# Optimization experiments

Measured on AMD Instinct MI355X. Metric: run time of the kernel, lower is better.

## Reference

```python
import jax, jax.numpy as jnp
import numpy as np

N_NODES = 100000
N_EDGES = 3200000
N_FEAT = 128
N_HID = 128
N_CLASS = 16
AVG_DEG = 32


def setup_inputs() -> dict:
    key = jax.random.key(0)
    ks = jax.random.split(key, 8)
    x = jax.random.normal(ks[0], (N_NODES, N_FEAT), dtype=jnp.float32)
    edge_row = jax.random.randint(ks[1], (N_EDGES,), 0, N_NODES, dtype=jnp.int32)
    edge_col = jax.random.randint(ks[2], (N_EDGES,), 0, N_NODES, dtype=jnp.int32)
    # normalized adjacency values ~ 1/degree
    edge_val = jax.random.uniform(ks[3], (N_EDGES,), dtype=jnp.float32) * (1.0 / AVG_DEG)
    W1 = jax.random.normal(ks[4], (N_FEAT, N_HID), dtype=jnp.float32) * (1.0 / np.sqrt(N_FEAT))
    b1 = jnp.zeros((N_HID,), dtype=jnp.float32)
    W4 = jax.random.normal(ks[5], (N_HID, N_CLASS), dtype=jnp.float32) * (1.0 / np.sqrt(N_HID))
    b4 = jnp.zeros((N_CLASS,), dtype=jnp.float32)
    return {"x": x, "edge_val": edge_val, "W1": W1, "b1": b1, "W4": W4, "b4": b4,
            "edge_row": edge_row, "edge_col": edge_col}


def _spmm(edge_val, edge_row, edge_col, feats, n_nodes):
    # sparse adj (COO) @ dense feats: gather source rows, scale, scatter-add to dest rows
    msgs = edge_val[:, None] * feats[edge_col]  # [E, D]
    return jax.ops.segment_sum(msgs, edge_row, num_segments=n_nodes)


def reference(x, edge_val, W1, b1, W4, b4, edge_row, edge_col):
    # gc1: adj @ (x @ W1) + b1, then ReLU (dropout is identity in eval mode)
    h = jax.nn.relu(_spmm(edge_val, edge_row, edge_col, x @ W1, N_NODES) + b1)
    # gc4: adj @ (h @ W4) + b4
    out = _spmm(edge_val, edge_row, edge_col, h @ W4, N_NODES) + b4
    return jax.nn.log_softmax(out, axis=1)
```

## Files before the change

### kernel.cpp

```cpp
#include <hip/hip_runtime.h>
#include <hip/hip_bf16.h>

constexpr int NN = 100000;
constexpr int NE = 3200000;
constexpr int NWG = 256;
constexpr int CHUNK = NE / NWG;
constexpr int CHUNK4 = CHUNK / 4;
constexpr int NBUK1 = (NN + 511) / 512;

__device__ __forceinline__ unsigned short f2bf(float f) {
    unsigned int u = __float_as_uint(f);
    unsigned int r = (u + 0x7fffu + ((u >> 16) & 1u)) >> 16;
    return (unsigned short)r;
}

__global__ __launch_bounds__(256) void k_gemm1(const float* __restrict__ x,
                                               const float* __restrict__ W,
                                               unsigned short* __restrict__ y) {
    __shared__ float ws_[128 * 128];
    __shared__ float xs[8][128];
    const int t = threadIdx.x;
    for (int i = t; i < 128 * 128; i += 256) ws_[i] = W[i];

    const int rowg = t >> 5;
    const int cq   = (t & 31) * 4;
    const int row0 = blockIdx.x * 32;

    for (int rs = 0; rs < 32; rs += 8) {
        __syncthreads();
        {
            const int r  = t >> 5;
            const int c4 = (t & 31) * 4;
            const int row = row0 + rs + r;
            float4 val = (row < NN) ? *(const float4*)(x + row * 128 + c4)
                                    : make_float4(0.f, 0.f, 0.f, 0.f);
            *(float4*)(&xs[r][c4]) = val;
        }
        __syncthreads();
        float4 acc = make_float4(0.f, 0.f, 0.f, 0.f);
#pragma unroll
        for (int k = 0; k < 128; ++k) {
            const float xv = xs[rowg][k];
            const float4 wv = *(const float4*)(&ws_[k * 128 + cq]);
            acc.x = fmaf(xv, wv.x, acc.x);
            acc.y = fmaf(xv, wv.y, acc.y);
            acc.z = fmaf(xv, wv.z, acc.z);
            acc.w = fmaf(xv, wv.w, acc.w);
        }
        const int row = row0 + rs + rowg;
        if (row < NN) {
            ushort4 o;
            o.x = f2bf(acc.x); o.y = f2bf(acc.y);
            o.z = f2bf(acc.z); o.w = f2bf(acc.w);
            *(ushort4*)(y + row * 128 + cq) = o;
        }
    }
}


__global__ __launch_bounds__(256) void k_count(const int4* __restrict__ erow4,
                                               int* __restrict__ cnt_tbl) {
    __shared__ int hist[NBUK1];
    const int t = threadIdx.x, wg = blockIdx.x;
    for (int i = t; i < NBUK1; i += 256) hist[i] = 0;
    __syncthreads();
    const int end4 = (wg + 1) * CHUNK4;
    for (int i4 = wg * CHUNK4 + t; i4 < end4; i4 += 256) {
        const int4 r = erow4[i4];
        atomicAdd(&hist[r.x >> 9], 1);
        atomicAdd(&hist[r.y >> 9], 1);
        atomicAdd(&hist[r.z >> 9], 1);
        atomicAdd(&hist[r.w >> 9], 1);
    }
    __syncthreads();
    for (int i = t; i < NBUK1; i += 256) cnt_tbl[wg * NBUK1 + i] = hist[i];
}

__global__ __launch_bounds__(256) void k_scan2(const int* __restrict__ cnt_tbl,
                                               int* __restrict__ off_tbl,
                                               int* __restrict__ boff) {
    __shared__ int sd[256];
    const int t = threadIdx.x;
    int tot = 0;
    if (t < NBUK1)
        for (int wg = 0; wg < NWG; ++wg) tot += cnt_tbl[wg * NBUK1 + t];
    sd[t] = tot;
    __syncthreads();
    for (int off = 1; off < 256; off <<= 1) {
        int a = sd[t];
        int b = (t >= off) ? sd[t - off] : 0;
        __syncthreads();
        sd[t] = a + b;
        __syncthreads();
    }
    const int base = sd[t] - tot;
    if (t < NBUK1) {
        boff[t] = base;
        int run = base;
        for (int wg = 0; wg < NWG; ++wg) {
            off_tbl[wg * NBUK1 + t] = run;
            run += cnt_tbl[wg * NBUK1 + t];
        }
    }
    if (t == 0) boff[NBUK1] = NE;
}

__global__ __launch_bounds__(256) void k_place(const int4* __restrict__ erow4,
                                               const int4* __restrict__ ecol4,
                                               const float4* __restrict__ eval4,
                                               const int* __restrict__ off_tbl,
                                               uint2* __restrict__ tmp) {
    __shared__ int cur[NBUK1];
    const int t = threadIdx.x, wg = blockIdx.x;
    for (int i = t; i < NBUK1; i += 256) cur[i] = off_tbl[wg * NBUK1 + i];
    __syncthreads();
    const int end4 = (wg + 1) * CHUNK4;
    for (int i4 = wg * CHUNK4 + t; i4 < end4; i4 += 256) {
        const int4 r = erow4[i4];
        const int4 c = ecol4[i4];
        const float4 v = eval4[i4];
        int p;
        p = atomicAdd(&cur[r.x >> 9], 1);
        tmp[p] = make_uint2(((unsigned)(r.x & 511) << 17) | (unsigned)c.x, __float_as_uint(v.x));
        p = atomicAdd(&cur[r.y >> 9], 1);
        tmp[p] = make_uint2(((unsigned)(r.y & 511) << 17) | (unsigned)c.y, __float_as_uint(v.y));
        p = atomicAdd(&cur[r.z >> 9], 1);
        tmp[p] = make_uint2(((unsigned)(r.z & 511) << 17) | (unsigned)c.z, __float_as_uint(v.z));
        p = atomicAdd(&cur[r.w >> 9], 1);
        tmp[p] = make_uint2(((unsigned)(r.w & 511) << 17) | (unsigned)c.w, __float_as_uint(v.w));
    }
}

__global__ __launch_bounds__(256) void k_sort2(const uint2* __restrict__ tmp,
                                               const int* __restrict__ boff,
                                               uint2* __restrict__ recs,
                                               int* __restrict__ row_start) {
    __shared__ int hist[512];
    __shared__ int cur[512];
    __shared__ int sd[256];
    const int b = blockIdx.x, t = threadIdx.x;
    const int base = boff[b];
    const int n = boff[b + 1] - base;
    hist[t] = 0; hist[t + 256] = 0;
    __syncthreads();
    for (int i = t; i < n; i += 256)
        atomicAdd(&hist[tmp[base + i].x >> 17], 1);
    __syncthreads();
    const int h0 = hist[2 * t], h1 = hist[2 * t + 1];
    const int pairsum = h0 + h1;
    sd[t] = pairsum;
    __syncthreads();
    for (int off = 1; off < 256; off <<= 1) {
        int a = sd[t];
        int bb = (t >= off) ? sd[t - off] : 0;
        __syncthreads();
        sd[t] = a + bb;
        __syncthreads();
    }
    const int e0 = sd[t] - pairsum;
    const int e1 = e0 + h0;
    cur[2 * t] = base + e0;
    cur[2 * t + 1] = base + e1;
    const int gr0 = b * 512 + 2 * t;
    if (gr0 < NN)     row_start[gr0] = base + e0;
    if (gr0 + 1 < NN) row_start[gr0 + 1] = base + e1;
    if (b == 0 && t == 0) row_start[NN] = NE;
    __syncthreads();
    for (int i = t; i < n; i += 256) {
        const uint2 rc = tmp[base + i];
        const int lr = rc.x >> 17;
        const int pos = atomicAdd(&cur[lr], 1);
        recs[pos] = make_uint2(rc.x & 0x1FFFFu, rc.y);
    }
}

__global__ __launch_bounds__(256) void k_spmm1(const unsigned int* __restrict__ xw1u,
                                               const int* __restrict__ row_start,
                                               const uint2* __restrict__ recs,
                                               const float* __restrict__ b1,
                                               float* __restrict__ h) {
    const int wid = (blockIdx.x * 256 + threadIdx.x) >> 6;
    const int lane = threadIdx.x & 63;
    if (wid >= NN) return;
    const int s = row_start[wid], e = row_start[wid + 1];
    float2 acc = make_float2(0.f, 0.f);
    for (int base = s; base < e; base += 64) {
        const int n = min(64, e - base);
        uint2 rv = make_uint2(0u, 0u);
        if (lane < n) rv = recs[base + lane];
        int j = 0;
        for (; j + 2 <= n; j += 2) {
            const int c0 = __shfl((int)rv.x, j), c1 = __shfl((int)rv.x, j + 1);
            const float v0 = __uint_as_float((unsigned int)__shfl((int)rv.y, j));
            const float v1 = __uint_as_float((unsigned int)__shfl((int)rv.y, j + 1));
            const unsigned int u0 = xw1u[c0 * 64 + lane];
            const unsigned int u1 = xw1u[c1 * 64 + lane];
            acc.x = fmaf(v0, __uint_as_float(u0 << 16), acc.x);
            acc.y = fmaf(v0, __uint_as_float(u0 & 0xffff0000u), acc.y);
            acc.x = fmaf(v1, __uint_as_float(u1 << 16), acc.x);
            acc.y = fmaf(v1, __uint_as_float(u1 & 0xffff0000u), acc.y);
        }
        if (j < n) {
            const int c0 = __shfl((int)rv.x, j);
            const float v0 = __uint_as_float((unsigned int)__shfl((int)rv.y, j));
            const unsigned int u0 = xw1u[c0 * 64 + lane];
            acc.x = fmaf(v0, __uint_as_float(u0 << 16), acc.x);
            acc.y = fmaf(v0, __uint_as_float(u0 & 0xffff0000u), acc.y);
        }
    }
    const float2 bb = *(const float2*)(b1 + (lane << 1));
    acc.x = fmaxf(acc.x + bb.x, 0.f);
    acc.y = fmaxf(acc.y + bb.y, 0.f);
    *(float2*)(h + wid * 128 + (lane << 1)) = acc;
}

__global__ __launch_bounds__(256) void k_gemm2(const float* __restrict__ h,
                                               const float* __restrict__ W4,
                                               unsigned short* __restrict__ y) {
    __shared__ float w4s[128 * 16];
    __shared__ float hs[16 * 132];
    const int t = threadIdx.x;
    for (int i = t; i < 128 * 16; i += 256) w4s[i] = W4[i];
    const int row0 = blockIdx.x * 16;
    for (int idx4 = t; idx4 < 512; idx4 += 256) {
        const int r = idx4 >> 5;
        const int c4 = (idx4 & 31) * 4;
        const int row = row0 + r;
        float4 v = (row < NN) ? *(const float4*)(h + row * 128 + c4)
                              : make_float4(0.f, 0.f, 0.f, 0.f);
        *(float4*)(&hs[r * 132 + c4]) = v;
    }
    __syncthreads();
    const int r = t >> 4, c = t & 15;
    float acc = 0.f;
#pragma unroll
    for (int k = 0; k < 128; ++k) acc = fmaf(hs[r * 132 + k], w4s[k * 16 + c], acc);
    const int row = row0 + r;
    if (row < NN) y[row * 16 + c] = f2bf(acc);
}

__global__ __launch_bounds__(256) void k_spmm2(const __hip_bfloat16* __restrict__ hw4,
                                               const int* __restrict__ row_start,
                                               const uint2* __restrict__ recs,
                                               const float* __restrict__ b4,
                                               float* __restrict__ out) {
    const int wid = (blockIdx.x * 256 + threadIdx.x) >> 6;
    const int lane = threadIdx.x & 63;
    if (wid >= NN) return;
    const int f = lane & 15, g = lane >> 4;
    const int s = row_start[wid], e = row_start[wid + 1];
    float acc = 0.f;
    for (int base = s + g; base < e; base += 4) {
        const uint2 rv = recs[base];
        const int c = (int)rv.x;
        const float v = __uint_as_float(rv.y);
        const float a = __uint_as_float(((unsigned int)*(const unsigned short*)(hw4 + c * 16 + f)) << 16);
        acc = fmaf(v, a, acc);
    }
    acc += __shfl_xor(acc, 16);
    acc += __shfl_xor(acc, 32);
    acc += b4[f];
    float m = acc;
#pragma unroll
    for (int off = 1; off < 16; off <<= 1) m = fmaxf(m, __shfl_xor(m, off));
    const float ex = __expf(acc - m);
    float sum = ex;
#pragma unroll
    for (int off = 1; off < 16; off <<= 1) sum += __shfl_xor(sum, off);
    const float res = acc - m - __logf(sum);
    if (lane < 16) out[wid * 16 + f] = res;
}

extern "C" void kernel_launch(void* const* d_in, const int* in_sizes, int n_in,
                              void* d_out, int out_size, void* d_ws, size_t ws_size,
                              hipStream_t stream) {
    const float* x        = (const float*)d_in[0];
    const float* edge_val = (const float*)d_in[1];
    const float* W1       = (const float*)d_in[2];
    const float* b1       = (const float*)d_in[3];
    const float* W4       = (const float*)d_in[4];
    const float* b4       = (const float*)d_in[5];
    const int*   edge_row = (const int*)d_in[6];
    const int*   edge_col = (const int*)d_in[7];
    float* out = (float*)d_out;

    char* ws = (char*)d_ws;
    size_t off = 0;
    auto alloc = [&](size_t bytes) -> void* {
        void* p = ws + off;
        off = (off + bytes + 255) & ~(size_t)255;
        return p;
    };
    unsigned short* xw1 = (unsigned short*)alloc((size_t)NN * 128 * 2);
    float* h            = (float*)alloc((size_t)NN * 128 * 4);
    unsigned short* hw4 = (unsigned short*)alloc((size_t)NN * 16 * 2);
    int*   cnt_tbl      = (int*)alloc((size_t)NWG * NBUK1 * 4);
    int*   off_tbl      = (int*)alloc((size_t)NWG * NBUK1 * 4);
    int*   boff         = (int*)alloc((size_t)(NBUK1 + 1) * 4);
    int*   row_start    = (int*)alloc((size_t)(NN + 1) * 4);
    uint2* tmp          = (uint2*)alloc((size_t)NE * 8);
    uint2* recs         = (uint2*)alloc((size_t)NE * 8);

    k_gemm1<<<NN / 32, 256, 0, stream>>>(x, W1, xw1);
    k_count<<<NWG, 256, 0, stream>>>((const int4*)edge_row, cnt_tbl);
    k_scan2<<<1, 256, 0, stream>>>(cnt_tbl, off_tbl, boff);
    k_place<<<NWG, 256, 0, stream>>>((const int4*)edge_row, (const int4*)edge_col,
                                     (const float4*)edge_val, off_tbl, tmp);
    k_sort2<<<NBUK1, 256, 0, stream>>>(tmp, boff, recs, row_start);
    k_spmm1<<<(NN + 3) / 4, 256, 0, stream>>>((const unsigned int*)xw1, row_start, recs, b1, h);
    k_gemm2<<<(NN + 15) / 16, 256, 0, stream>>>(h, W4, hw4);
    k_spmm2<<<(NN + 3) / 4, 256, 0, stream>>>((const __hip_bfloat16*)hw4, row_start, recs, b4, out);
}
```

Measured before the change: 526.1 us.

## Fuse h@W4 into spmm1 epilogue and stage sort buckets in LDS

Removes the separate k_gemm2 kernel and the fp32 h buffer: each wave in spmm1 now multiplies its finished ReLU row by W4 held in padded shared memory and writes the bf16 hw4 row directly. This avoids writing and re-reading a 51 MB intermediate. The bucket sort is also changed to 256-row buckets so each k_sort2 block can cache its records in LDS instead of reading tmp from global memory twice, and the scan is adjusted for 391 buckets. The cost is extra shared-memory use (about 72 KB in sort2) and a W4 load per spmm1 block, both of which may lower occupancy.

```diff
diff --git a/kernel.cpp b/kernel.cpp
--- a/kernel.cpp
+++ b/kernel.cpp
@@ -6,7 +6,9 @@
 constexpr int NWG = 256;
 constexpr int CHUNK = NE / NWG;
 constexpr int CHUNK4 = CHUNK / 4;
-constexpr int NBUK1 = (NN + 511) / 512;
+constexpr int ROWS_B = 256;
+constexpr int NBUK1 = (NN + ROWS_B - 1) / ROWS_B;
+constexpr int SORT_CAP = 9216;
 
 __device__ __forceinline__ unsigned short f2bf(float f) {
     unsigned int u = __float_as_uint(f);
@@ -67,10 +69,10 @@
     const int end4 = (wg + 1) * CHUNK4;
     for (int i4 = wg * CHUNK4 + t; i4 < end4; i4 += 256) {
         const int4 r = erow4[i4];
-        atomicAdd(&hist[r.x >> 9], 1);
-        atomicAdd(&hist[r.y >> 9], 1);
-        atomicAdd(&hist[r.z >> 9], 1);
-        atomicAdd(&hist[r.w >> 9], 1);
+        atomicAdd(&hist[r.x >> 8], 1);
+        atomicAdd(&hist[r.y >> 8], 1);
+        atomicAdd(&hist[r.z >> 8], 1);
+        atomicAdd(&hist[r.w >> 8], 1);
     }
     __syncthreads();
     for (int i = t; i < NBUK1; i += 256) cnt_tbl[wg * NBUK1 + i] = hist[i];
@@ -81,9 +83,10 @@
                                                int* __restrict__ boff) {
     __shared__ int sd[256];
     const int t = threadIdx.x;
+    const int b0 = 2 * t, b1 = 2 * t + 1;
     int tot = 0;
-    if (t < NBUK1)
-        for (int wg = 0; wg < NWG; ++wg) tot += cnt_tbl[wg * NBUK1 + t];
+    if (b0 < NBUK1) for (int wg = 0; wg < NWG; ++wg) tot += cnt_tbl[wg * NBUK1 + b0];
+    if (b1 < NBUK1) for (int wg = 0; wg < NWG; ++wg) tot += cnt_tbl[wg * NBUK1 + b1];
     sd[t] = tot;
     __syncthreads();
     for (int off = 1; off < 256; off <<= 1) {
@@ -93,16 +96,22 @@
         sd[t] = a + b;
         __syncthreads();
     }
-    const int base = sd[t] - tot;
-    if (t < NBUK1) {
-        boff[t] = base;
-        int run = base;
+    int run = sd[t] - tot;
+    if (b0 < NBUK1) {
+        boff[b0] = run;
         for (int wg = 0; wg < NWG; ++wg) {
-            off_tbl[wg * NBUK1 + t] = run;
-            run += cnt_tbl[wg * NBUK1 + t];
-        }
-    }
-    if (t == 0) boff[NBUK1] = NE;
+            off_tbl[wg * NBUK1 + b0] = run;
+            run += cnt_tbl[wg * NBUK1 + b0];
+        }
+    }
+    if (b1 < NBUK1) {
+        boff[b1] = run;
+        for (int wg = 0; wg < NWG; ++wg) {
+            off_tbl[wg * NBUK1 + b1] = run;
+            run += cnt_tbl[wg * NBUK1 + b1];
+        }
+    }
+    if (t == 255) boff[NBUK1] = NE;
 }
 
 __global__ __launch_bounds__(256) void k_place(const int4* __restrict__ erow4,
@@ -120,14 +129,14 @@
         const int4 c = ecol4[i4];
         const float4 v = eval4[i4];
         int p;
-        p = atomicAdd(&cur[r.x >> 9], 1);
-        tmp[p] = make_uint2(((unsigned)(r.x & 511) << 17) | (unsigned)c.x, __float_as_uint(v.x));
-        p = atomicAdd(&cur[r.y >> 9], 1);
-        tmp[p] = make_uint2(((unsigned)(r.y & 511) << 17) | (unsigned)c.y, __float_as_uint(v.y));
-        p = atomicAdd(&cur[r.z >> 9], 1);
-        tmp[p] = make_uint2(((unsigned)(r.z & 511) << 17) | (unsigned)c.z, __float_as_uint(v.z));
-        p = atomicAdd(&cur[r.w >> 9], 1);
-        tmp[p] = make_uint2(((unsigned)(r.w & 511) << 17) | (unsigned)c.w, __float_as_uint(v.w));
+        p = atomicAdd(&cur[r.x >> 8], 1);
+        tmp[p] = make_uint2(((unsigned)(r.x & 255) << 17) | (unsigned)c.x, __float_as_uint(v.x));
+        p = atomicAdd(&cur[r.y >> 8], 1);
+        tmp[p] = make_uint2(((unsigned)(r.y & 255) << 17) | (unsigned)c.y, __float_as_uint(v.y));
+        p = atomicAdd(&cur[r.z >> 8], 1);
+        tmp[p] = make_uint2(((unsigned)(r.z & 255) << 17) | (unsigned)c.z, __float_as_uint(v.z));
+        p = atomicAdd(&cur[r.w >> 8], 1);
+        tmp[p] = make_uint2(((unsigned)(r.w & 255) << 17) | (unsigned)c.w, __float_as_uint(v.w));
     }
 }
 
@@ -135,20 +144,23 @@
                                                const int* __restrict__ boff,
                                                uint2* __restrict__ recs,
                                                int* __restrict__ row_start) {
-    __shared__ int hist[512];
-    __shared__ int cur[512];
+    __shared__ uint2 sbuf[SORT_CAP];
+    __shared__ int hist[ROWS_B];
+    __shared__ int cur[ROWS_B];
     __shared__ int sd[256];
     const int b = blockIdx.x, t = threadIdx.x;
     const int base = boff[b];
     const int n = boff[b + 1] - base;
-    hist[t] = 0; hist[t + 256] = 0;
-    __syncthreads();
-    for (int i = t; i < n; i += 256)
-        atomicAdd(&hist[tmp[base + i].x >> 17], 1);
-    __syncthreads();
-    const int h0 = hist[2 * t], h1 = hist[2 * t + 1];
-    const int pairsum = h0 + h1;
-    sd[t] = pairsum;
+    hist[t] = 0;
+    __syncthreads();
+    for (int i = t; i < n; i += 256) {
+        const uint2 rc = tmp[base + i];
+        if (i < SORT_CAP) sbuf[i] = rc;
+        atomicAdd(&hist[rc.x >> 17], 1);
+    }
+    __syncthreads();
+    const int hv = hist[t];
+    sd[t] = hv;
     __syncthreads();
     for (int off = 1; off < 256; off <<= 1) {
         int a = sd[t];
@@ -157,17 +169,14 @@
         sd[t] = a + bb;
         __syncthreads();
     }
-    const int e0 = sd[t] - pairsum;
-    const int e1 = e0 + h0;
-    cur[2 * t] = base + e0;
-    cur[2 * t + 1] = base + e1;
-    const int gr0 = b * 512 + 2 * t;
-    if (gr0 < NN)     row_start[gr0] = base + e0;
-    if (gr0 + 1 < NN) row_start[gr0 + 1] = base + e1;
-    if (b == 0 && t == 0) row_start[NN] = NE;
+    const int excl = sd[t] - hv;
+    cur[t] = base + excl;
+    const int gr = b * ROWS_B + t;
+    if (gr < NN) row_start[gr] = base + excl;
+    if (b == NBUK1 - 1 && t == 0) row_start[NN] = NE;
     __syncthreads();
     for (int i = t; i < n; i += 256) {
-        const uint2 rc = tmp[base + i];
+        const uint2 rc = (i < SORT_CAP) ? sbuf[i] : tmp[base + i];
         const int lr = rc.x >> 17;
         const int pos = atomicAdd(&cur[lr], 1);
         recs[pos] = make_uint2(rc.x & 0x1FFFFu, rc.y);
@@ -178,9 +187,19 @@
                                                const int* __restrict__ row_start,
                                                const uint2* __restrict__ recs,
                                                const float* __restrict__ b1,
-                                               float* __restrict__ h) {
-    const int wid = (blockIdx.x * 256 + threadIdx.x) >> 6;
-    const int lane = threadIdx.x & 63;
+                                               const float* __restrict__ W4,
+                                               unsigned short* __restrict__ hw4) {
+    __shared__ float w4p[2048 + 48];
+    __shared__ float hrow[4][132];
+    const int t = threadIdx.x;
+    for (int i = t; i < 2048; i += 256) {
+        const int k = i >> 4;
+        w4p[i + 16 * (k >> 5)] = W4[i];
+    }
+    __syncthreads();
+
+    const int wid = (blockIdx.x * 256 + t) >> 6;
+    const int lane = t & 63;
     if (wid >= NN) return;
     const int s = row_start[wid], e = row_start[wid + 1];
     float2 acc = make_float2(0.f, 0.f);
@@ -211,32 +230,19 @@
     const float2 bb = *(const float2*)(b1 + (lane << 1));
     acc.x = fmaxf(acc.x + bb.x, 0.f);
     acc.y = fmaxf(acc.y + bb.y, 0.f);
-    *(float2*)(h + wid * 128 + (lane << 1)) = acc;
-}
-
-__global__ __launch_bounds__(256) void k_gemm2(const float* __restrict__ h,
-                                               const float* __restrict__ W4,
-                                               unsigned short* __restrict__ y) {
-    __shared__ float w4s[128 * 16];
-    __shared__ float hs[16 * 132];
-    const int t = threadIdx.x;
-    for (int i = t; i < 128 * 16; i += 256) w4s[i] = W4[i];
-    const int row0 = blockIdx.x * 16;
-    for (int idx4 = t; idx4 < 512; idx4 += 256) {
-        const int r = idx4 >> 5;
-        const int c4 = (idx4 & 31) * 4;
-        const int row = row0 + r;
-        float4 v = (row < NN) ? *(const float4*)(h + row * 128 + c4)
-                              : make_float4(0.f, 0.f, 0.f, 0.f);
-        *(float4*)(&hs[r * 132 + c4]) = v;
-    }
-    __syncthreads();
-    const int r = t >> 4, c = t & 15;
-    float acc = 0.f;
+
+    const int wv = t >> 6;
+    *(float2*)(&hrow[wv][2 * lane + (lane >> 4)]) = acc;
+    const int q = lane >> 4, c = lane & 15;
+    float p = 0.f;
 #pragma unroll
-    for (int k = 0; k < 128; ++k) acc = fmaf(hs[r * 132 + k], w4s[k * 16 + c], acc);
-    const int row = row0 + r;
-    if (row < NN) y[row * 16 + c] = f2bf(acc);
+    for (int j = 0; j < 32; ++j) {
+        const int k = 32 * q + j;
+        p = fmaf(hrow[wv][k + q], w4p[16 * k + c + 16 * q], p);
+    }
+    p += __shfl_xor(p, 16);
+    p += __shfl_xor(p, 32);
+    if (lane < 16) hw4[wid * 16 + c] = f2bf(p);
 }
 
 __global__ __launch_bounds__(256) void k_spmm2(const __hip_bfloat16* __restrict__ hw4,
@@ -292,7 +298,6 @@
         return p;
     };
     unsigned short* xw1 = (unsigned short*)alloc((size_t)NN * 128 * 2);
-    float* h            = (float*)alloc((size_t)NN * 128 * 4);
     unsigned short* hw4 = (unsigned short*)alloc((size_t)NN * 16 * 2);
     int*   cnt_tbl      = (int*)alloc((size_t)NWG * NBUK1 * 4);
     int*   off_tbl      = (int*)alloc((size_t)NWG * NBUK1 * 4);
@@ -307,7 +312,7 @@
     k_place<<<NWG, 256, 0, stream>>>((const int4*)edge_row, (const int4*)edge_col,
                                      (const float4*)edge_val, off_tbl, tmp);
     k_sort2<<<NBUK1, 256, 0, stream>>>(tmp, boff, recs, row_start);
-    k_spmm1<<<(NN + 3) / 4, 256, 0, stream>>>((const unsigned int*)xw1, row_start, recs, b1, h);
-    k_gemm2<<<(NN + 15) / 16, 256, 0, stream>>>(h, W4, hw4);
+    k_spmm1<<<(NN + 3) / 4, 256, 0, stream>>>((const unsigned int*)xw1, row_start, recs,
+                                              b1, W4, hw4);
     k_spmm2<<<(NN + 3) / 4, 256, 0, stream>>>((const __hip_bfloat16*)hw4, row_start, recs, b4, out);
 }
```

Result: no change. 536.4 us (+2.0%).
